# Performance work log

Hardware: AMD Instinct MI355X
Metric: run time of the kernel (lower is better)

The kernel has to match this reference:

```python
import jax, jax.numpy as jnp
import numpy as np

NUM_BLOCKS = 2
NUM_LAYERS = 10
L = NUM_BLOCKS * NUM_LAYERS  # 20 wave layers
C_IN, C_RES, C_SKIP = 8, 64, 256
B, T = 32, 4096


def causal_conv1d(x, w, b, dilation=1):
    # x: [B, C_in, T], w: [C_out, C_in, K], left-pad so output is causal and length-preserving
    k = w.shape[2]
    out = jax.lax.conv_general_dilated(
        x, w, window_strides=(1,), padding=[(dilation * (k - 1), 0)],
        rhs_dilation=(dilation,), dimension_numbers=("NCH", "OIH", "NCH"))
    return out + b[None, :, None]


def setup_inputs() -> dict:
    key = jax.random.key(0)
    ks = jax.random.split(key, 12)
    s1 = 1.0 / np.sqrt(C_IN)
    s2 = 1.0 / np.sqrt(2 * C_RES)
    s3 = 1.0 / np.sqrt(C_RES)
    return {
        "x":    jax.random.normal(ks[0], (B, C_IN, T), jnp.float32),
        "w_in": jax.random.normal(ks[1], (C_RES, C_IN, 1), jnp.float32) * s1,
        "b_in": jax.random.normal(ks[2], (C_RES,), jnp.float32) * s1,
        "w_f":  jax.random.normal(ks[3], (L, C_RES, C_RES, 2), jnp.float32) * s2,
        "b_f":  jax.random.normal(ks[4], (L, C_RES), jnp.float32) * s2,
        "w_g":  jax.random.normal(ks[5], (L, C_RES, C_RES, 2), jnp.float32) * s2,
        "b_g":  jax.random.normal(ks[6], (L, C_RES), jnp.float32) * s2,
        "w_s":  jax.random.normal(ks[7], (L, C_SKIP, C_RES, 1), jnp.float32) * s3,
        "b_s":  jax.random.normal(ks[8], (L, C_SKIP), jnp.float32) * s3,
        "w_r":  jax.random.normal(ks[9], (L, C_RES, C_RES, 1), jnp.float32) * s3,
        "b_r":  jax.random.normal(ks[10], (L, C_RES), jnp.float32) * s3,
    }


def reference(x, w_in, b_in, w_f, b_f, w_g, b_g, w_s, b_s, w_r, b_r):
    # WaveNet.encode: 1x1 input conv, then num_blocks*num_layers gated dilated causal layers
    h = causal_conv1d(x, w_in, b_in)            # [B, C_RES, T]
    skips = jnp.zeros((x.shape[0], w_s.shape[1], x.shape[2]), x.dtype)
    for i in range(L):
        d = 2 ** (i % NUM_LAYERS)
        f = jnp.tanh(causal_conv1d(h, w_f[i], b_f[i], d))
        g = jax.nn.sigmoid(causal_conv1d(h, w_g[i], b_g[i], d))
        z = f * g                                # gated activation
        skips = skips + causal_conv1d(z, w_s[i], b_s[i])
        h = h + causal_conv1d(z, w_r[i], b_r[i])  # residual connection
    return skips
```

## Files before the change

### kernel.cpp

```cpp
#include <hip/hip_runtime.h>

#define B_ 32
#define T_ 4096
#define CR 64
#define CS 256
#define NL 20

typedef __bf16 bf16x8 __attribute__((ext_vector_type(8)));
typedef __bf16 bf16x4v __attribute__((ext_vector_type(4)));
typedef float f32x4 __attribute__((ext_vector_type(4)));

__device__ __forceinline__ f32x4 mfma16(bf16x8 a, bf16x8 b, f32x4 c) {
  return __builtin_amdgcn_mfma_f32_16x16x32_bf16(a, b, c, 0, 0, 0);
}

__global__ void pack_kernel(const float* __restrict__ wf, const float* __restrict__ wg,
                            const float* __restrict__ wsn, const float* __restrict__ wr,
                            const float* __restrict__ bs,
                            __bf16* __restrict__ Wfg2, __bf16* __restrict__ Wr2,
                            __bf16* __restrict__ Ws2, float* __restrict__ bsS) {
  int n = blockIdx.x * 256 + threadIdx.x;
  if (n < 327680) {
    int j = n & 7, lane = (n >> 3) & 63, fr = (n >> 9) & 7, mt = (n >> 12) & 3, i = n >> 14;
    int cs = mt * 16 + (lane & 15);
    int k = (fr & 3) * 32 + (lane >> 4) * 8 + j;
    int ci = k & 63, tap = k >> 6;
    const float* src = (fr < 4) ? wf : wg;
    Wfg2[n] = (__bf16)src[((i * 64 + cs) * 64 + ci) * 2 + tap];
  } else if (n < 409600) {
    int m = n - 327680;
    int j = m & 7, lane = (m >> 3) & 63, kc = (m >> 9) & 1, mt = (m >> 10) & 3, i = m >> 12;
    int cs = mt * 16 + (lane & 15);
    int ci = kc * 32 + (lane >> 4) * 8 + j;
    Wr2[m] = (__bf16)wr[(i * 64 + cs) * 64 + ci];
  } else if (n < 737280) {
    int m = n - 409600;
    int j = m & 7, lane = (m >> 3) & 63, kc = (m >> 9) & 1, tile = (m >> 10) & 15, i = m >> 14;
    int cs = tile * 16 + (lane & 15);
    int ci = kc * 32 + (lane >> 4) * 8 + j;
    Ws2[m] = (__bf16)wsn[i * 16384 + cs * 64 + ci];
  } else if (n < 737536) {
    int cs = n - 737280;
    float s = 0.f;
    for (int i = 0; i < NL; ++i) s += bs[i * 256 + cs];
    bsS[cs] = s;
  }
}

__global__ void inconv_kernel(const float* __restrict__ x, const float* __restrict__ w_in,
                              const float* __restrict__ b_in, float* __restrict__ h0) {
  __shared__ float w[64][8];
  __shared__ float bi[64];
  int tid = threadIdx.x;
  for (int k = tid; k < 512; k += 256) w[k >> 3][k & 7] = w_in[k];
  if (tid < 64) bi[tid] = b_in[tid];
  __syncthreads();
  int b = blockIdx.x >> 4;
  int t = ((blockIdx.x & 15) << 8) + tid;
  float xv[8];
#pragma unroll
  for (int ci = 0; ci < 8; ++ci) xv[ci] = x[((size_t)b * 8 + ci) * T_ + t];
  float* orow = h0 + ((size_t)b * T_ + t) * 64;
#pragma unroll
  for (int c0 = 0; c0 < 64; c0 += 4) {
    float s0 = bi[c0], s1 = bi[c0 + 1], s2 = bi[c0 + 2], s3 = bi[c0 + 3];
#pragma unroll
    for (int ci = 0; ci < 8; ++ci) {
      s0 += w[c0][ci] * xv[ci];
      s1 += w[c0 + 1][ci] * xv[ci];
      s2 += w[c0 + 2][ci] * xv[ci];
      s3 += w[c0 + 3][ci] * xv[ci];
    }
    float4 o = make_float4(s0, s1, s2, s3);
    *(float4*)(orow + c0) = o;
  }
}

__global__ __launch_bounds__(256) void layer_kernel(
    const float* __restrict__ h_in, float* __restrict__ h_out,
    const __bf16* __restrict__ Wfg, const __bf16* __restrict__ Wr,
    const float* __restrict__ bF, const float* __restrict__ bG,
    const float* __restrict__ bR,
    __bf16* __restrict__ Zg, int d, int il, int Gs) {
  __shared__ __bf16 sB[2][64][72];

  const int tid = threadIdx.x;
  const int b = blockIdx.x >> 6;
  const int t0 = (blockIdx.x & 63) << 6;
  const float* hbase = h_in + ((size_t)b * T_ + t0) * 64;

#pragma unroll
  for (int it = 0; it < 4; ++it) {
    int f = (it * 256 + tid) * 4;
    int tr = f >> 6, c = f & 63;
    float4 v = *(const float4*)(hbase + tr * 64 + c);
    bf16x4v pc = {(__bf16)v.x, (__bf16)v.y, (__bf16)v.z, (__bf16)v.w};
    *(bf16x4v*)&sB[1][tr][c] = pc;
    int td = t0 + tr - d;
    float4 u = make_float4(0.f, 0.f, 0.f, 0.f);
    if (td >= 0) u = *(const float4*)(h_in + ((size_t)b * T_ + td) * 64 + c);
    bf16x4v pd = {(__bf16)u.x, (__bf16)u.y, (__bf16)u.z, (__bf16)u.w};
    *(bf16x4v*)&sB[0][tr][c] = pd;
  }
  __syncthreads();

  const int lane = tid & 63, wid = tid >> 6;
  const int tl = (wid << 4) | (lane & 15);
  const int kq = lane >> 4;

  bf16x8 bh[4];
  bh[0] = *(const bf16x8*)&sB[0][tl][kq * 8];
  bh[1] = *(const bf16x8*)&sB[0][tl][32 + kq * 8];
  bh[2] = *(const bf16x8*)&sB[1][tl][kq * 8];
  bh[3] = *(const bf16x8*)&sB[1][tl][32 + kq * 8];

  __bf16 (*sZ)[72] = sB[0];

#pragma unroll
  for (int mt = 0; mt < 4; ++mt) {
    const __bf16* wb = Wfg + (mt * 8) * 512 + lane * 8;
    f32x4 aF = {0.f, 0.f, 0.f, 0.f}, aG = {0.f, 0.f, 0.f, 0.f};
#pragma unroll
    for (int kc = 0; kc < 4; ++kc) {
      aF = mfma16(*(const bf16x8*)(wb + kc * 512), bh[kc], aF);
      aG = mfma16(*(const bf16x8*)(wb + (4 + kc) * 512), bh[kc], aG);
    }
    const int c0 = (mt << 4) + (kq << 2);
    float4 bfv = *(const float4*)(bF + c0);
    float4 bgv = *(const float4*)(bG + c0);
    float fb[4] = {bfv.x, bfv.y, bfv.z, bfv.w};
    float gb[4] = {bgv.x, bgv.y, bgv.z, bgv.w};
    bf16x4v zv;
#pragma unroll
    for (int r = 0; r < 4; ++r) {
      float fp = aF[r] + fb[r];
      float gp = aG[r] + gb[r];
      float e = __expf(2.f * fp);
      float th = 1.f - 2.f / (e + 1.f);
      float sg = 1.f / (1.f + __expf(-gp));
      zv[r] = (__bf16)(th * sg);
    }
    *(bf16x4v*)&sZ[tl][c0] = zv;
  }

  bf16x8 bz0 = *(const bf16x8*)&sZ[tl][kq * 8];
  bf16x8 bz1 = *(const bf16x8*)&sZ[tl][32 + kq * 8];
#pragma unroll
  for (int mt = 0; mt < 4; ++mt) {
    const __bf16* wrb = Wr + (mt * 2) * 512 + lane * 8;
    f32x4 aR = {0.f, 0.f, 0.f, 0.f};
    aR = mfma16(*(const bf16x8*)(wrb), bz0, aR);
    aR = mfma16(*(const bf16x8*)(wrb + 512), bz1, aR);
    const int c0 = (mt << 4) + (kq << 2);
    float4 hv = *(const float4*)(h_in + ((size_t)b * T_ + t0 + tl) * 64 + c0);
    float4 brv = *(const float4*)(bR + c0);
    float4 o;
    o.x = hv.x + aR[0] + brv.x;
    o.y = hv.y + aR[1] + brv.y;
    o.z = hv.z + aR[2] + brv.z;
    o.w = hv.w + aR[3] + brv.w;
    *(float4*)(h_out + ((size_t)b * T_ + t0 + tl) * 64 + c0) = o;
  }

  __syncthreads();
  {
    int tr = tid >> 2, ch = (tid & 3) << 4;
    const uint4 v0 = *(const uint4*)&sZ[tr][ch];
    const uint4 v1 = *(const uint4*)&sZ[tr][ch + 8];
    __bf16* dst = Zg + (((size_t)b * T_ + t0 + tr) * Gs + il) * 64 + ch;
    *(uint4*)dst = v0;
    *(uint4*)(dst + 8) = v1;
  }
}

__global__ __launch_bounds__(256) void skip_kernel(
    const __bf16* __restrict__ Zg, const __bf16* __restrict__ Ws2,
    const float* __restrict__ bsS, float* __restrict__ out,
    int i0, int cnt, int Gs, int first) {
  __shared__ __bf16 sZ[2][64][72];

  const int tid = threadIdx.x;
  const int b = blockIdx.x >> 6;
  const int t0 = (blockIdx.x & 63) << 6;
  const int lane = tid & 63, wid = tid >> 6;
  const int kq = lane >> 4;
  const int tr = tid >> 2, coff = (tid & 3) << 4;

  const __bf16* zbase = Zg + (((size_t)b * T_ + t0 + tr) * Gs) * 64 + coff;
  const __bf16* wbase = Ws2 + (size_t)i0 * 16384 + (size_t)(wid * 8) * 512 + lane * 8;

  {
    uint4 z0 = *(const uint4*)zbase;
    uint4 z1 = *(const uint4*)(zbase + 8);
    *(uint4*)&sZ[0][tr][coff] = z0;
    *(uint4*)&sZ[0][tr][coff + 8] = z1;
  }
  bf16x8 aw[8];
#pragma unroll
  for (int f = 0; f < 8; ++f) aw[f] = *(const bf16x8*)(wbase + f * 512);

  f32x4 acc[16];
#pragma unroll
  for (int q = 0; q < 16; ++q) acc[q] = (f32x4){0.f, 0.f, 0.f, 0.f};

  __syncthreads();

  const char* zrow0 = (const char*)&sZ[0][0][0] + (lane & 15) * 144 + kq * 16;

  for (int il = 0; il < cnt; ++il) {
    const int cur = il & 1;
    bf16x8 bz[8];
#pragma unroll
    for (int nt = 0; nt < 4; ++nt) {
      bz[nt * 2]     = *(const bf16x8*)(zrow0 + cur * 9216 + nt * 2304);
      bz[nt * 2 + 1] = *(const bf16x8*)(zrow0 + cur * 9216 + nt * 2304 + 64);
    }
    uint4 p0, p1;
    bf16x8 awn[8];
    const bool more = (il + 1) < cnt;
    if (more) {
      p0 = *(const uint4*)(zbase + (il + 1) * 64);
      p1 = *(const uint4*)(zbase + (il + 1) * 64 + 8);
#pragma unroll
      for (int f = 0; f < 8; ++f)
        awn[f] = *(const bf16x8*)(wbase + (size_t)(il + 1) * 16384 + f * 512);
    }
#pragma unroll
    for (int mt = 0; mt < 4; ++mt) {
#pragma unroll
      for (int nt = 0; nt < 4; ++nt) {
        acc[mt * 4 + nt] = mfma16(aw[mt * 2], bz[nt * 2], acc[mt * 4 + nt]);
        acc[mt * 4 + nt] = mfma16(aw[mt * 2 + 1], bz[nt * 2 + 1], acc[mt * 4 + nt]);
      }
    }
    if (more) {
      *(uint4*)&sZ[cur ^ 1][tr][coff] = p0;
      *(uint4*)&sZ[cur ^ 1][tr][coff + 8] = p1;
#pragma unroll
      for (int f = 0; f < 8; ++f) aw[f] = awn[f];
      __syncthreads();
    }
  }

  const int csb = wid * 64 + (kq << 2);
  const int tcol = t0 + (lane & 15);
#pragma unroll
  for (int mt = 0; mt < 4; ++mt) {
#pragma unroll
    for (int nt = 0; nt < 4; ++nt) {
#pragma unroll
      for (int r = 0; r < 4; ++r) {
        int cs = csb + mt * 16 + r;
        size_t idx = ((size_t)b * CS + cs) * T_ + tcol + nt * 16;
        float v = acc[mt * 4 + nt][r];
        if (first) out[idx] = v + bsS[cs];
        else out[idx] += v;
      }
    }
  }
}

extern "C" void kernel_launch(void* const* d_in, const int* in_sizes, int n_in,
                              void* d_out, int out_size, void* d_ws, size_t ws_size,
                              hipStream_t stream) {
  (void)in_sizes; (void)n_in; (void)out_size;
  const float* x    = (const float*)d_in[0];
  const float* w_in = (const float*)d_in[1];
  const float* b_in = (const float*)d_in[2];
  const float* w_f  = (const float*)d_in[3];
  const float* b_f  = (const float*)d_in[4];
  const float* w_g  = (const float*)d_in[5];
  const float* b_g  = (const float*)d_in[6];
  const float* w_s  = (const float*)d_in[7];
  const float* b_s  = (const float*)d_in[8];
  const float* w_r  = (const float*)d_in[9];
  const float* b_r  = (const float*)d_in[10];
  float* out = (float*)d_out;

  char* ws = (char*)d_ws;
  size_t off = 0;
  auto alloc = [&](size_t bytes) -> char* {
    char* p = ws + off;
    off = (off + bytes + 255) & ~(size_t)255;
    return p;
  };
  float* hA = (float*)alloc((size_t)B_ * T_ * 64 * 4);
  float* hB = (float*)alloc((size_t)B_ * T_ * 64 * 4);
  __bf16* Wfg2 = (__bf16*)alloc((size_t)NL * 16384 * 2);
  __bf16* Wr2  = (__bf16*)alloc((size_t)NL * 4096 * 2);
  __bf16* Ws2  = (__bf16*)alloc((size_t)NL * 16384 * 2);
  float* bsS = (float*)alloc(CS * 4);

  size_t zslot = (size_t)B_ * T_ * 64 * 2;
  size_t rem = (ws_size > off) ? (ws_size - off) : 0;
  int G = (int)(rem / zslot);
  if (G > NL) G = NL;
  if (G < 1) G = 1;
  __bf16* Zg = (__bf16*)(ws + off);

  hipLaunchKernelGGL(pack_kernel, dim3(2881), dim3(256), 0, stream,
                     w_f, w_g, w_s, w_r, b_s, Wfg2, Wr2, Ws2, bsS);
  hipLaunchKernelGGL(inconv_kernel, dim3(512), dim3(256), 0, stream, x, w_in, b_in, hA);

  float* hc = hA;
  float* hn = hB;
  int i0 = 0;
  for (int i = 0; i < NL; ++i) {
    int il = i - i0;
    hipLaunchKernelGGL(layer_kernel, dim3(B_ * 64), dim3(256), 0, stream,
                       hc, hn, Wfg2 + (size_t)i * 16384, Wr2 + (size_t)i * 4096,
                       b_f + i * 64, b_g + i * 64, b_r + i * 64,
                       Zg, 1 << (i % 10), il, G);
    { float* tmp = hc; hc = hn; hn = tmp; }
    if (il + 1 == G || i == NL - 1) {
      int cnt = il + 1;
      hipLaunchKernelGGL(skip_kernel, dim3(B_ * 64), dim3(256), 0, stream,
                         Zg, Ws2, bsS, out, i0, cnt, G, (i0 == 0) ? 1 : 0);
      i0 = i + 1;
    }
  }
}
```

Before: 1.004 ms.

## Store gated activations in MFMA fragment order and double layer-kernel time tile

The layer kernel now processes 128 timesteps per block, with two N-tiles per wave, so each weight fragment is reused across two MFMAs. It also writes the Z activations to global memory already in per-lane MFMA B-fragment order. The skip kernel can then load the fragments directly from global into registers, which removes its shared-memory staging and per-layer barriers. The cost is half as many layer blocks, more registers per thread and twice the LDS per block, which could reduce occupancy.

```diff
diff --git a/kernel.cpp b/kernel.cpp
--- a/kernel.cpp
+++ b/kernel.cpp
@@ -82,15 +82,16 @@
     const float* __restrict__ bF, const float* __restrict__ bG,
     const float* __restrict__ bR,
     __bf16* __restrict__ Zg, int d, int il, int Gs) {
-  __shared__ __bf16 sB[2][64][72];
+  __shared__ __bf16 sB[2][128][72];
 
   const int tid = threadIdx.x;
-  const int b = blockIdx.x >> 6;
-  const int t0 = (blockIdx.x & 63) << 6;
+  const int b = blockIdx.x >> 5;
+  const int tb = blockIdx.x & 31;
+  const int t0 = tb << 7;
   const float* hbase = h_in + ((size_t)b * T_ + t0) * 64;
 
 #pragma unroll
-  for (int it = 0; it < 4; ++it) {
+  for (int it = 0; it < 8; ++it) {
     int f = (it * 256 + tid) * 4;
     int tr = f >> 6, c = f & 63;
     float4 v = *(const float4*)(hbase + tr * 64 + c);
@@ -105,71 +106,99 @@
   __syncthreads();
 
   const int lane = tid & 63, wid = tid >> 6;
-  const int tl = (wid << 4) | (lane & 15);
+  const int rb = wid << 5;
   const int kq = lane >> 4;
 
-  bf16x8 bh[4];
-  bh[0] = *(const bf16x8*)&sB[0][tl][kq * 8];
-  bh[1] = *(const bf16x8*)&sB[0][tl][32 + kq * 8];
-  bh[2] = *(const bf16x8*)&sB[1][tl][kq * 8];
-  bh[3] = *(const bf16x8*)&sB[1][tl][32 + kq * 8];
+  bf16x8 bh[2][4];
+#pragma unroll
+  for (int nt = 0; nt < 2; ++nt) {
+    int tl = rb + (nt << 4) + (lane & 15);
+    bh[nt][0] = *(const bf16x8*)&sB[0][tl][kq * 8];
+    bh[nt][1] = *(const bf16x8*)&sB[0][tl][32 + kq * 8];
+    bh[nt][2] = *(const bf16x8*)&sB[1][tl][kq * 8];
+    bh[nt][3] = *(const bf16x8*)&sB[1][tl][32 + kq * 8];
+  }
 
   __bf16 (*sZ)[72] = sB[0];
 
 #pragma unroll
   for (int mt = 0; mt < 4; ++mt) {
     const __bf16* wb = Wfg + (mt * 8) * 512 + lane * 8;
-    f32x4 aF = {0.f, 0.f, 0.f, 0.f}, aG = {0.f, 0.f, 0.f, 0.f};
+    f32x4 aF[2] = {{0.f, 0.f, 0.f, 0.f}, {0.f, 0.f, 0.f, 0.f}};
+    f32x4 aG[2] = {{0.f, 0.f, 0.f, 0.f}, {0.f, 0.f, 0.f, 0.f}};
 #pragma unroll
     for (int kc = 0; kc < 4; ++kc) {
-      aF = mfma16(*(const bf16x8*)(wb + kc * 512), bh[kc], aF);
-      aG = mfma16(*(const bf16x8*)(wb + (4 + kc) * 512), bh[kc], aG);
+      bf16x8 af = *(const bf16x8*)(wb + kc * 512);
+      bf16x8 ag = *(const bf16x8*)(wb + (4 + kc) * 512);
+#pragma unroll
+      for (int nt = 0; nt < 2; ++nt) {
+        aF[nt] = mfma16(af, bh[nt][kc], aF[nt]);
+        aG[nt] = mfma16(ag, bh[nt][kc], aG[nt]);
+      }
     }
     const int c0 = (mt << 4) + (kq << 2);
     float4 bfv = *(const float4*)(bF + c0);
     float4 bgv = *(const float4*)(bG + c0);
     float fb[4] = {bfv.x, bfv.y, bfv.z, bfv.w};
     float gb[4] = {bgv.x, bgv.y, bgv.z, bgv.w};
-    bf16x4v zv;
-#pragma unroll
-    for (int r = 0; r < 4; ++r) {
-      float fp = aF[r] + fb[r];
-      float gp = aG[r] + gb[r];
-      float e = __expf(2.f * fp);
-      float th = 1.f - 2.f / (e + 1.f);
-      float sg = 1.f / (1.f + __expf(-gp));
-      zv[r] = (__bf16)(th * sg);
-    }
-    *(bf16x4v*)&sZ[tl][c0] = zv;
-  }
-
-  bf16x8 bz0 = *(const bf16x8*)&sZ[tl][kq * 8];
-  bf16x8 bz1 = *(const bf16x8*)&sZ[tl][32 + kq * 8];
+#pragma unroll
+    for (int nt = 0; nt < 2; ++nt) {
+      bf16x4v zv;
+#pragma unroll
+      for (int r = 0; r < 4; ++r) {
+        float fp = aF[nt][r] + fb[r];
+        float gp = aG[nt][r] + gb[r];
+        float e = __expf(2.f * fp);
+        float th = 1.f - 2.f / (e + 1.f);
+        float sg = 1.f / (1.f + __expf(-gp));
+        zv[r] = (__bf16)(th * sg);
+      }
+      *(bf16x4v*)&sZ[rb + (nt << 4) + (lane & 15)][c0] = zv;
+    }
+  }
+
+  bf16x8 bz[2][2];
+#pragma unroll
+  for (int nt = 0; nt < 2; ++nt) {
+    int tl = rb + (nt << 4) + (lane & 15);
+    bz[nt][0] = *(const bf16x8*)&sZ[tl][kq * 8];
+    bz[nt][1] = *(const bf16x8*)&sZ[tl][32 + kq * 8];
+  }
 #pragma unroll
   for (int mt = 0; mt < 4; ++mt) {
     const __bf16* wrb = Wr + (mt * 2) * 512 + lane * 8;
-    f32x4 aR = {0.f, 0.f, 0.f, 0.f};
-    aR = mfma16(*(const bf16x8*)(wrb), bz0, aR);
-    aR = mfma16(*(const bf16x8*)(wrb + 512), bz1, aR);
+    bf16x8 ar0 = *(const bf16x8*)(wrb);
+    bf16x8 ar1 = *(const bf16x8*)(wrb + 512);
     const int c0 = (mt << 4) + (kq << 2);
-    float4 hv = *(const float4*)(h_in + ((size_t)b * T_ + t0 + tl) * 64 + c0);
     float4 brv = *(const float4*)(bR + c0);
-    float4 o;
-    o.x = hv.x + aR[0] + brv.x;
-    o.y = hv.y + aR[1] + brv.y;
-    o.z = hv.z + aR[2] + brv.z;
-    o.w = hv.w + aR[3] + brv.w;
-    *(float4*)(h_out + ((size_t)b * T_ + t0 + tl) * 64 + c0) = o;
+#pragma unroll
+    for (int nt = 0; nt < 2; ++nt) {
+      f32x4 aR = {0.f, 0.f, 0.f, 0.f};
+      aR = mfma16(ar0, bz[nt][0], aR);
+      aR = mfma16(ar1, bz[nt][1], aR);
+      const int tl = rb + (nt << 4) + (lane & 15);
+      const float* hrow = h_in + ((size_t)b * T_ + t0 + tl) * 64 + c0;
+      float4 hv = *(const float4*)hrow;
+      float4 o;
+      o.x = hv.x + aR[0] + brv.x;
+      o.y = hv.y + aR[1] + brv.y;
+      o.z = hv.z + aR[2] + brv.z;
+      o.w = hv.w + aR[3] + brv.w;
+      *(float4*)(h_out + ((size_t)b * T_ + t0 + tl) * 64 + c0) = o;
+    }
   }
 
   __syncthreads();
-  {
-    int tr = tid >> 2, ch = (tid & 3) << 4;
-    const uint4 v0 = *(const uint4*)&sZ[tr][ch];
-    const uint4 v1 = *(const uint4*)&sZ[tr][ch + 8];
-    __bf16* dst = Zg + (((size_t)b * T_ + t0 + tr) * Gs + il) * 64 + ch;
-    *(uint4*)dst = v0;
-    *(uint4*)(dst + 8) = v1;
+#pragma unroll
+  for (int q = 0; q < 4; ++q) {
+    int g = q * 256 + tid;
+    int sub = g >> 9, cc = g & 511;
+    int nt2 = cc >> 7, kc2 = (cc >> 6) & 1, ln = cc & 63;
+    int row = sub * 64 + nt2 * 16 + (ln & 15);
+    int col = kc2 * 32 + (ln >> 4) * 8;
+    uint4 v = *(const uint4*)&sZ[row][col];
+    __bf16* dst = Zg + (((size_t)(b * 64 + tb * 2 + sub)) * Gs + il) * 4096 + cc * 8;
+    *(uint4*)dst = v;
   }
 }
 
@@ -177,53 +206,38 @@
     const __bf16* __restrict__ Zg, const __bf16* __restrict__ Ws2,
     const float* __restrict__ bsS, float* __restrict__ out,
     int i0, int cnt, int Gs, int first) {
-  __shared__ __bf16 sZ[2][64][72];
-
   const int tid = threadIdx.x;
   const int b = blockIdx.x >> 6;
-  const int t0 = (blockIdx.x & 63) << 6;
+  const int tt = blockIdx.x & 63;
+  const int t0 = tt << 6;
   const int lane = tid & 63, wid = tid >> 6;
   const int kq = lane >> 4;
-  const int tr = tid >> 2, coff = (tid & 3) << 4;
-
-  const __bf16* zbase = Zg + (((size_t)b * T_ + t0 + tr) * Gs) * 64 + coff;
-  const __bf16* wbase = Ws2 + (size_t)i0 * 16384 + (size_t)(wid * 8) * 512 + lane * 8;
-
-  {
-    uint4 z0 = *(const uint4*)zbase;
-    uint4 z1 = *(const uint4*)(zbase + 8);
-    *(uint4*)&sZ[0][tr][coff] = z0;
-    *(uint4*)&sZ[0][tr][coff + 8] = z1;
-  }
-  bf16x8 aw[8];
-#pragma unroll
-  for (int f = 0; f < 8; ++f) aw[f] = *(const bf16x8*)(wbase + f * 512);
+
+  const __bf16* zb = Zg + ((size_t)(b * 64 + tt) * Gs) * 4096 + lane * 8;
+  const __bf16* wb = Ws2 + (size_t)i0 * 16384 + (size_t)(wid * 8) * 512 + lane * 8;
 
   f32x4 acc[16];
 #pragma unroll
   for (int q = 0; q < 16; ++q) acc[q] = (f32x4){0.f, 0.f, 0.f, 0.f};
 
-  __syncthreads();
-
-  const char* zrow0 = (const char*)&sZ[0][0][0] + (lane & 15) * 144 + kq * 16;
+  bf16x8 bz[8], aw[8];
+#pragma unroll
+  for (int f = 0; f < 8; ++f) {
+    bz[f] = *(const bf16x8*)(zb + f * 512);
+    aw[f] = *(const bf16x8*)(wb + f * 512);
+  }
 
   for (int il = 0; il < cnt; ++il) {
-    const int cur = il & 1;
-    bf16x8 bz[8];
-#pragma unroll
-    for (int nt = 0; nt < 4; ++nt) {
-      bz[nt * 2]     = *(const bf16x8*)(zrow0 + cur * 9216 + nt * 2304);
-      bz[nt * 2 + 1] = *(const bf16x8*)(zrow0 + cur * 9216 + nt * 2304 + 64);
-    }
-    uint4 p0, p1;
-    bf16x8 awn[8];
+    bf16x8 bzn[8], awn[8];
     const bool more = (il + 1) < cnt;
     if (more) {
-      p0 = *(const uint4*)(zbase + (il + 1) * 64);
-      p1 = *(const uint4*)(zbase + (il + 1) * 64 + 8);
-#pragma unroll
-      for (int f = 0; f < 8; ++f)
-        awn[f] = *(const bf16x8*)(wbase + (size_t)(il + 1) * 16384 + f * 512);
+      const __bf16* zb2 = zb + (size_t)(il + 1) * 4096;
+      const __bf16* wb2 = wb + (size_t)(il + 1) * 16384;
+#pragma unroll
+      for (int f = 0; f < 8; ++f) {
+        bzn[f] = *(const bf16x8*)(zb2 + f * 512);
+        awn[f] = *(const bf16x8*)(wb2 + f * 512);
+      }
     }
 #pragma unroll
     for (int mt = 0; mt < 4; ++mt) {
@@ -234,11 +248,11 @@
       }
     }
     if (more) {
-      *(uint4*)&sZ[cur ^ 1][tr][coff] = p0;
-      *(uint4*)&sZ[cur ^ 1][tr][coff + 8] = p1;
-#pragma unroll
-      for (int f = 0; f < 8; ++f) aw[f] = awn[f];
-      __syncthreads();
+#pragma unroll
+      for (int f = 0; f < 8; ++f) {
+        bz[f] = bzn[f];
+        aw[f] = awn[f];
+      }
     }
   }
 
@@ -307,7 +321,7 @@
   int i0 = 0;
   for (int i = 0; i < NL; ++i) {
     int il = i - i0;
-    hipLaunchKernelGGL(layer_kernel, dim3(B_ * 64), dim3(256), 0, stream,
+    hipLaunchKernelGGL(layer_kernel, dim3(B_ * 32), dim3(256), 0, stream,
                        hc, hn, Wfg2 + (size_t)i * 16384, Wr2 + (size_t)i * 4096,
                        b_f + i * 64, b_g + i * 64, b_r + i * 64,
                        Zg, 1 << (i % 10), il, G);
```

New measurement: 1.014 ms. Within noise of the previous version (+1.0%).
